# Kernel tuning notes

Hardware: AMD Instinct MI355X
Metric: run time of the kernel (lower is better)

The kernel has to match this reference:

```python
import jax, jax.numpy as jnp
import numpy as np

B, T, D, H, V = 32, 1024, 768, 1024, 30522
TAU_RANK, GAMMA_RANK, TAU_GATE = 0.05, 2.0, 0.2
RHOS = (0.1, 0.25, 0.5)


def setup_inputs() -> dict:
    key = jax.random.key(0)
    ks = jax.random.split(key, 6)
    ids = jax.random.randint(ks[0], (B, T), 0, V, dtype=jnp.int32)
    embeddings = jax.random.normal(ks[1], (B, T, D), dtype=jnp.float32)
    attn = jax.random.randint(ks[2], (B, T), 0, 2, dtype=jnp.int32)
    return {
        'ids': ids,
        'embeddings': embeddings,
        'attn': attn,
        'ln_g': jnp.ones((D,), jnp.float32),
        'ln_b': jnp.zeros((D,), jnp.float32),
        'w1': jax.random.normal(ks[3], (D, H), jnp.float32) * 0.02,
        'b1': jnp.zeros((H,), jnp.float32),
        'w2': jax.random.normal(ks[4], (H, 1), jnp.float32) * 0.02,
        'b2': jnp.zeros((1,), jnp.float32),
        'emb_table': jax.random.normal(ks[5], (V, D), jnp.float32) * 0.02,
    }


def _layer_norm(x, g, b, eps=1e-5):
    mu = x.mean(-1, keepdims=True)
    var = ((x - mu) ** 2).mean(-1, keepdims=True)
    return (x - mu) * jax.lax.rsqrt(var + eps) * g + b


def _selector(x, ln_g, ln_b, w1, b1, w2, b2):
    # SelectorMLP (dropout in eval mode): LN -> Linear -> exact GELU -> Linear -> squeeze
    h = _layer_norm(x, ln_g, ln_b)
    h = jax.nn.gelu(h @ w1 + b1, approximate=False)
    return (h @ w2 + b2)[..., 0]  # [B,T]


def _soft_rank(scores, attn_f, tau, gamma):
    scores = jnp.where(attn_f == 0, 0.0, scores)
    denom = jnp.clip(attn_f.sum(1, keepdims=True), 1.0, None)
    mean = (scores * attn_f).sum(1, keepdims=True) / denom
    var = (((scores - mean) ** 2) * attn_f).sum(1, keepdims=True) / denom
    scores = (scores - mean) / jnp.sqrt(var + 1e-6)
    # diff[b,i,j] = scores[b,j] - scores[b,i]
    diff = scores[:, None, :] - scores[:, :, None]
    p = jax.nn.sigmoid(diff / tau) ** gamma
    p = p * attn_f[:, None, :]
    r = 1.0 + p.sum(axis=1)  # [B,T]
    return jnp.where(attn_f == 0, 1e9, r)


def _pool(tok, w):
    # masked weighted mean pooling (stub of sent_encoder.pool)
    return (tok * w[:, :, None]).sum(1) / jnp.clip(w.sum(1), 1e-9, None)[:, None]


def reference(ids, embeddings, attn, ln_g, ln_b, w1, b1, w2, b2, emb_table):
    attn_f = attn.astype(jnp.float32)
    emb = embeddings * attn_f[..., None]
    scores = _selector(emb, ln_g, ln_b, w1, b1, w2, b2)
    scores = jnp.where(attn_f == 0, 0.0, scores)

    tok_full = emb_table[ids]  # stub sent_encoder.token_embeddings
    full_rep = jax.lax.stop_gradient(_pool(tok_full, attn_f))  # torch.no_grad()

    T_eff = attn_f.sum(1)
    ranks = _soft_rank(scores, attn_f, TAU_RANK, GAMMA_RANK)
    # position of each token in ascending rank order; padded tokens (rank 1e9) sort last
    pos = jnp.argsort(jnp.argsort(ranks, axis=1), axis=1)

    recon_sum = jnp.zeros((), jnp.float32)
    hard_masks, rho_effs, losses = [], [], []
    for rho in RHOS:
        k = jnp.maximum(jnp.round(rho * T_eff), 1.0)  # per-batch variable k
        gate_raw = jax.nn.sigmoid((k[:, None] - ranks) / TAU_GATE) * attn_f
        g_soft = gate_raw / jnp.clip(gate_raw.sum(1, keepdims=True), 1e-8, None) * k[:, None]
        # batched equivalent of the per-row topk(-ranks, kb) scatter loop
        hard_mask = (pos < k[:, None]).astype(jnp.float32)
        k_eff = g_soft.sum(1)
        rho_eff = k_eff / jnp.clip(T_eff, 1.0, None)
        effective_attn = attn_f * g_soft
        pred_rep = _pool(emb_table[ids], effective_attn)
        l_r = jnp.mean((pred_rep - full_rep) ** 2)  # recon_loss stub (MSE)
        recon_sum = recon_sum + l_r
        hard_masks.append(hard_mask)
        rho_effs.append(rho_eff)
        losses.append(l_r)
    recon_avg = recon_sum / len(RHOS)
    return (g_soft, jnp.stack(hard_masks), recon_avg, jnp.stack(losses), jnp.stack(rho_effs))
```

## Files before the change

### kernel.cpp

```cpp
#include <hip/hip_runtime.h>
#include <math.h>

#define BT 32768
#define Dd 768
#define Hh 1024
#define Bb 32
#define Tt 1024
#define MT_CAP 17152
#define MTILE_CAP 134

typedef __bf16 bf16x8 __attribute__((ext_vector_type(8)));
typedef float f32x4 __attribute__((ext_vector_type(4)));

#define GL2LDS16(gp, lp) __builtin_amdgcn_global_load_lds( \
    (const __attribute__((address_space(1))) void*)(gp),   \
    (__attribute__((address_space(3))) void*)(lp), 16, 0, 0)

__device__ __forceinline__ float block_reduce_sum_256(float v, float* red4) {
    int tid = threadIdx.x;
    #pragma unroll
    for (int o = 32; o > 0; o >>= 1) v += __shfl_down(v, o);
    __syncthreads();
    if ((tid & 63) == 0) red4[tid >> 6] = v;
    __syncthreads();
    return red4[0] + red4[1] + red4[2] + red4[3];
}

__device__ __forceinline__ void bf16split(float x, short& h, short& l) {
    unsigned u = __float_as_uint(x);
    unsigned r = (u + 0x7FFFu + ((u >> 16) & 1u)) >> 16;
    h = (short)r;
    float fh = __uint_as_float(r << 16);
    float lof = x - fh;
    unsigned u2 = __float_as_uint(lof);
    unsigned r2 = (u2 + 0x7FFFu + ((u2 >> 16) & 1u)) >> 16;
    l = (short)r2;
}

__device__ __forceinline__ int pack2(short a, short b) {
    return (int)(unsigned short)a | ((int)(unsigned short)b << 16);
}

__global__ __launch_bounds__(256) void seg_count_kernel(
    const int* __restrict__ attn, int* __restrict__ segsum)
{
    const int tid = threadIdx.x;
    int a = (attn[blockIdx.x * 256 + tid] != 0) ? 1 : 0;
    #pragma unroll
    for (int o = 32; o > 0; o >>= 1) a += __shfl_down(a, o);
    __shared__ int w4[4];
    if ((tid & 63) == 0) w4[tid >> 6] = a;
    __syncthreads();
    if (tid == 0) segsum[blockIdx.x] = w4[0] + w4[1] + w4[2] + w4[3];
}

__global__ __launch_bounds__(256) void cidx_kernel(
    const int* __restrict__ attn, const int* __restrict__ segsum,
    const float* __restrict__ b2,
    int* __restrict__ row_of, int* __restrict__ tok_of,
    float* __restrict__ scores, float* __restrict__ teff, int* __restrict__ mh)
{
    __shared__ int sbase[128];
    __shared__ int w0tot;
    __shared__ int wcnt[4];
    const int bid = blockIdx.x, tid = threadIdx.x;

    int v = 0, s = 0;
    if (tid < 128) {
        const int ln = tid & 63;
        v = segsum[tid];
        s = v;
        #pragma unroll
        for (int o = 1; o < 64; o <<= 1) {
            int t = __shfl_up(s, o);
            if (ln >= o) s += t;
        }
        if (tid == 63) w0tot = s;
    }
    __syncthreads();
    if (tid < 128) {
        int base = (tid >= 64) ? w0tot : 0;
        sbase[tid] = base + s - v;
        if (tid == 127 && bid == 0) mh[0] = base + s;
    }
    if (tid == 0 && (bid & 3) == 0)
        teff[bid >> 2] = (float)(segsum[bid] + segsum[bid + 1] +
                                 segsum[bid + 2] + segsum[bid + 3]);

    const int tok = bid * 256 + tid;
    const int active = (attn[tok] != 0) ? 1 : 0;
    unsigned long long m = __ballot(active);
    const int lane = tid & 63, wv = tid >> 6;
    if (lane == 0) wcnt[wv] = __popcll(m);
    __syncthreads();
    int woff = 0;
    for (int q = 0; q < wv; ++q) woff += wcnt[q];
    int below = __popcll(m & ((1ULL << lane) - 1ULL));
    int row = sbase[bid] + woff + below;
    row_of[tok] = active ? row : -1;
    if (active) tok_of[row] = tok;
    scores[tok] = active ? b2[0] : 0.f;
}

__global__ __launch_bounds__(256) void prep_kernel(
    const float* __restrict__ w1,
    short* __restrict__ w1t_hi, short* __restrict__ w1t_lo,
    const float* __restrict__ emb, const int* __restrict__ attn,
    const int* __restrict__ row_of,
    const float* __restrict__ ln_g, const float* __restrict__ ln_b,
    short* __restrict__ a_hi, short* __restrict__ a_lo)
{
    __shared__ float tile[32][65];
    const int bid = blockIdx.x, tid = threadIdx.x;

    if (bid < 384) {
        const int kb  = bid % 24;
        const int nb0 = (bid / 24) * 64;
        const int r0 = tid >> 6, c = tid & 63;
        #pragma unroll
        for (int rr = 0; rr < 8; ++rr) {
            int k = kb * 32 + r0 + rr * 4;
            tile[r0 + rr * 4][c] = w1[(size_t)k * 1024 + nb0 + c];
        }
        __syncthreads();
        const int n = tid >> 2, kc = (tid & 3) * 8;
        short h[8], lo[8];
        #pragma unroll
        for (int e = 0; e < 8; ++e) bf16split(tile[kc + e][n], h[e], lo[e]);
        size_t off = (size_t)(nb0 + n) * 768 + kb * 32 + kc;
        *(int4*)(w1t_hi + off) = make_int4(pack2(h[0],h[1]), pack2(h[2],h[3]),
                                           pack2(h[4],h[5]), pack2(h[6],h[7]));
        *(int4*)(w1t_lo + off) = make_int4(pack2(lo[0],lo[1]), pack2(lo[2],lo[3]),
                                           pack2(lo[4],lo[5]), pack2(lo[6],lo[7]));
        return;
    }

    int tok  = (bid - 384) * 4 + (tid >> 6);
    int lane = tid & 63;
    int av   = attn[tok];
    if (av == 0) return;
    int row = row_of[tok];
    if (row >= MT_CAP) return;
    float af = (float)av;
    const float4* row4 = (const float4*)(emb + (size_t)tok * Dd);
    float4 x[3];
    #pragma unroll
    for (int e = 0; e < 3; ++e) x[e] = row4[lane + 64 * e];
    float s = 0.f;
    #pragma unroll
    for (int e = 0; e < 3; ++e) {
        x[e].x *= af; x[e].y *= af; x[e].z *= af; x[e].w *= af;
        s += x[e].x + x[e].y + x[e].z + x[e].w;
    }
    #pragma unroll
    for (int o = 32; o > 0; o >>= 1) s += __shfl_down(s, o);
    s = __shfl(s, 0);
    float mean = s / 768.0f;
    float q = 0.f;
    #pragma unroll
    for (int e = 0; e < 3; ++e) {
        float d0 = x[e].x - mean, d1 = x[e].y - mean, d2 = x[e].z - mean, d3 = x[e].w - mean;
        q += d0*d0 + d1*d1 + d2*d2 + d3*d3;
    }
    #pragma unroll
    for (int o = 32; o > 0; o >>= 1) q += __shfl_down(q, o);
    q = __shfl(q, 0);
    float rstd = 1.0f / sqrtf(q / 768.0f + 1e-5f);

    #pragma unroll
    for (int e = 0; e < 3; ++e) {
        int idx = lane * 4 + e * 256;
        float4 g4 = *(const float4*)(ln_g + idx);
        float4 b4 = *(const float4*)(ln_b + idx);
        float o0 = (x[e].x - mean) * rstd * g4.x + b4.x;
        float o1 = (x[e].y - mean) * rstd * g4.y + b4.y;
        float o2 = (x[e].z - mean) * rstd * g4.z + b4.z;
        float o3 = (x[e].w - mean) * rstd * g4.w + b4.w;
        short h0,h1,h2,h3,l0,l1,l2,l3;
        bf16split(o0,h0,l0); bf16split(o1,h1,l1);
        bf16split(o2,h2,l2); bf16split(o3,h3,l3);
        *(int2*)(a_hi + (size_t)row * 768 + idx) = make_int2(pack2(h0,h1), pack2(h2,h3));
        *(int2*)(a_lo + (size_t)row * 768 + idx) = make_int2(pack2(l0,l1), pack2(l2,l3));
    }
}

__global__ __launch_bounds__(512, 4) void score_gemm_mfma(
    const __bf16* __restrict__ a_hi, const __bf16* __restrict__ a_lo,
    const __bf16* __restrict__ w1t_hi, const __bf16* __restrict__ w1t_lo,
    const float* __restrict__ b1, const float* __restrict__ w2,
    const int* __restrict__ mh, const int* __restrict__ tok_of,
    float* __restrict__ scores)
{
    const int Mh = mh[0];
    int MtAct = (Mh + 127) >> 7;
    if (MtAct > MTILE_CAP) MtAct = MTILE_CAP;
    const int MtPad8 = (MtAct + 7) & ~7;
    const int njobs  = MtPad8 * 8;
    const int job = blockIdx.x;
    if (job >= njobs) return;
    const int mt = job % MtPad8;
    const int m0 = mt * 128;
    if (m0 >= Mh) return;
    const int nc = job / MtPad8;
    const int nb = nc * 128;

    __shared__ __align__(16) __bf16 sAh[2][8][512];
    __shared__ __align__(16) __bf16 sAl[2][8][512];
    __shared__ __align__(16) __bf16 sBh[2][8][512];
    __shared__ __align__(16) __bf16 sBl[2][8][512];

    const int tid = threadIdx.x;
    const int l   = tid & 63;
    const int w   = tid >> 6;
    const int rsel = l & 15;
    const int ksel = (l >> 4) * 8;
    const int wr   = w >> 2, wc = w & 3;

    const size_t aA = (size_t)(m0 + w * 16 + rsel) * 768 + ksel;
    const size_t aB = (size_t)(nb + w * 16 + rsel) * 768 + ksel;

    f32x4 acc[4][2];
    #pragma unroll
    for (int i = 0; i < 4; ++i)
        #pragma unroll
        for (int j = 0; j < 2; ++j) acc[i][j] = (f32x4){0.f, 0.f, 0.f, 0.f};

    auto stage = [&](int buf, int k0) {
        GL2LDS16(a_hi   + aA + k0, &sAh[buf][w][0]);
        GL2LDS16(a_lo   + aA + k0, &sAl[buf][w][0]);
        GL2LDS16(w1t_hi + aB + k0, &sBh[buf][w][0]);
        GL2LDS16(w1t_lo + aB + k0, &sBl[buf][w][0]);
    };

    stage(0, 0);

    for (int kt = 0; kt < 24; ++kt) {
        const int cur = kt & 1;
        __syncthreads();
        if (kt < 23) stage(cur ^ 1, (kt + 1) * 32);

        bf16x8 ah[4], al[4], bh[2], bl[2];
        #pragma unroll
        for (int mi = 0; mi < 4; ++mi) {
            ah[mi] = *(const bf16x8*)&sAh[cur][wr * 4 + mi][l * 8];
            al[mi] = *(const bf16x8*)&sAl[cur][wr * 4 + mi][l * 8];
        }
        #pragma unroll
        for (int ni = 0; ni < 2; ++ni) {
            bh[ni] = *(const bf16x8*)&sBh[cur][wc * 2 + ni][l * 8];
            bl[ni] = *(const bf16x8*)&sBl[cur][wc * 2 + ni][l * 8];
        }
        #pragma unroll
        for (int mi = 0; mi < 4; ++mi)
            #pragma unroll
            for (int ni = 0; ni < 2; ++ni)
                acc[mi][ni] = __builtin_amdgcn_mfma_f32_16x16x32_bf16(ah[mi], bh[ni], acc[mi][ni], 0, 0, 0);
        #pragma unroll
        for (int mi = 0; mi < 4; ++mi)
            #pragma unroll
            for (int ni = 0; ni < 2; ++ni)
                acc[mi][ni] = __builtin_amdgcn_mfma_f32_16x16x32_bf16(al[mi], bh[ni], acc[mi][ni], 0, 0, 0);
        #pragma unroll
        for (int mi = 0; mi < 4; ++mi)
            #pragma unroll
            for (int ni = 0; ni < 2; ++ni)
                acc[mi][ni] = __builtin_amdgcn_mfma_f32_16x16x32_bf16(ah[mi], bl[ni], acc[mi][ni], 0, 0, 0);
    }

    const int colbase = nb + wc * 32 + (l & 15);
    const int rowg    = (l >> 4) * 4;
    #pragma unroll
    for (int mi = 0; mi < 4; ++mi) {
        float v[4] = {0.f, 0.f, 0.f, 0.f};
        #pragma unroll
        for (int ni = 0; ni < 2; ++ni) {
            int col = colbase + ni * 16;
            float b1v = b1[col], w2v = w2[col];
            #pragma unroll
            for (int j = 0; j < 4; ++j) {
                float x = acc[mi][ni][j] + b1v;
                float g = 0.5f * x * (1.0f + erff(x * 0.70710678118654752440f));
                v[j] = fmaf(g, w2v, v[j]);
            }
        }
        #pragma unroll
        for (int j = 0; j < 4; ++j) {
            v[j] += __shfl_xor(v[j], 1);
            v[j] += __shfl_xor(v[j], 2);
            v[j] += __shfl_xor(v[j], 4);
            v[j] += __shfl_xor(v[j], 8);
        }
        if ((l & 15) == 0) {
            int rowb = m0 + wr * 64 + mi * 16 + rowg;
            #pragma unroll
            for (int j = 0; j < 4; ++j) {
                int row = rowb + j;
                if (row < Mh) atomicAdd(&scores[tok_of[row]], v[j]);
            }
        }
    }
}

__global__ __launch_bounds__(256) void rank_kernel(
    const float* __restrict__ scores, const int* __restrict__ attn,
    float* __restrict__ ranks, int* __restrict__ pos, float* __restrict__ gpart)
{
    __shared__ float sn[1024];
    __shared__ float afs[1024];
    __shared__ double dsum[256];
    __shared__ int    csum[256];
    __shared__ float  red4[4];
    const int b = blockIdx.x >> 5, qc = blockIdx.x & 31;
    const int tid = threadIdx.x;

    float sv[4], av[4];
    float sa = 0.f, ss = 0.f;
    #pragma unroll
    for (int e = 0; e < 4; ++e) {
        int i = tid + 256 * e;
        float af = (float)attn[b * 1024 + i];
        float s  = (af != 0.f) ? scores[b * 1024 + i] : 0.f;
        sn[i]  = s;
        afs[i] = af;
        sv[e] = s; av[e] = af;
        sa += af; ss += s;
    }
    float tot_a = block_reduce_sum_256(sa, red4);
    float tot_s = block_reduce_sum_256(ss, red4);
    float denom = fmaxf(tot_a, 1.0f);
    float mean  = tot_s / denom;
    float q = 0.f;
    #pragma unroll
    for (int e = 0; e < 4; ++e) { float d = sv[e] - mean; q += d * d * av[e]; }
    float tot_q = block_reduce_sum_256(q, red4);
    float rinv  = 1.0f / sqrtf(tot_q / denom + 1e-6f);

    #pragma unroll
    for (int e = 0; e < 4; ++e) {
        int i = tid + 256 * e;
        sn[i] = (sn[i] - mean) * rinv;
    }
    __syncthreads();

    const int jj  = tid & 31;
    const int grp = tid >> 5;
    const int j   = qc * 32 + jj;
    const float sj = sn[j];
    const bool  aj = (afs[j] != 0.f);
    double sum = 0.0;
    int    cnt = 0;
    const int i0 = grp * 128;
    #pragma unroll 4
    for (int i = i0; i < i0 + 128; ++i) {
        float si = sn[i];
        float ai = afs[i];
        float d   = (sj - si) * 20.0f;
        float e   = __expf(-d);
        float sig = 1.0f / (1.0f + e);
        sum += (double)(sig * sig);
        bool c;
        if (ai != 0.f) c = aj ? (si < sj || (si == sj && i < j)) : true;
        else           c = aj ? false : (i < j);
        cnt += c ? 1 : 0;
    }
    dsum[tid] = sum; csum[tid] = cnt;
    __syncthreads();
    if (tid < 32) {
        double s2 = 0.0; int c2 = 0;
        #pragma unroll
        for (int g = 0; g < 8; ++g) { s2 += dsum[tid + 32 * g]; c2 += csum[tid + 32 * g]; }
        const int jt = qc * 32 + tid;
        const int gj = b * 1024 + jt;
        const float af = afs[jt];
        const float rk = (af == 0.f) ? 1e9f : (float)(1.0 + s2);
        ranks[gj] = rk;
        pos[gj]   = c2;
        const float rhos[3] = {0.1f, 0.25f, 0.5f};
        #pragma unroll
        for (int r = 0; r < 3; ++r) {
            float k = fmaxf(rintf(rhos[r] * tot_a), 1.0f);
            float d = (k - rk) * 5.0f;
            float g = (1.0f / (1.0f + __expf(-d))) * af;
            #pragma unroll
            for (int o = 16; o > 0; o >>= 1) g += __shfl_xor(g, o);
            if (tid == 0) gpart[b * 96 + r * 32 + qc] = g;
        }
    }
}

__global__ __launch_bounds__(256) void gate_pool_kernel(
    const int* __restrict__ ids, const int* __restrict__ attn,
    const float* __restrict__ emb_table,
    const float* __restrict__ ranks, const int* __restrict__ pos,
    const float* __restrict__ gpart, const float* __restrict__ teff_v,
    float* __restrict__ keff, float* __restrict__ ppart, float* __restrict__ out)
{
    __shared__ float gpl[96];
    __shared__ float gsL[3][64];
    const int b = blockIdx.x >> 4, chunk = blockIdx.x & 15;
    const int tid = threadIdx.x;
    const int t0 = chunk * 64;
    const float teff = teff_v[b];

    if (tid < 96) gpl[tid] = gpart[b * 96 + tid];
    __syncthreads();

    const float rhos[3] = {0.1f, 0.25f, 0.5f};
    float kk[3], gsum[3], scale[3];
    #pragma unroll
    for (int r = 0; r < 3; ++r) {
        float s = 0.f;
        #pragma unroll
        for (int c = 0; c < 32; ++c) s += gpl[r * 32 + c];
        gsum[r]  = s;
        kk[r]    = fmaxf(rintf(rhos[r] * teff), 1.0f);
        scale[r] = kk[r] / fmaxf(s, 1e-8f);
    }

    if (tid < 192) {
        const int r = tid >> 6, t = tid & 63;
        const int gj = b * 1024 + t0 + t;
        const float rk = ranks[gj];
        const float af = (float)attn[gj];
        float d    = (kk[r] - rk) * 5.0f;
        float gate = (1.0f / (1.0f + __expf(-d))) * af;
        float gs   = gate * scale[r];
        gsL[r][t] = gs;
        out[BT + r * BT + gj] = ((float)pos[gj] < kk[r]) ? 1.0f : 0.0f;
        if (r == 2) out[gj] = gs;
    }
    if (chunk == 0 && tid == 0) {
        #pragma unroll
        for (int r = 0; r < 3; ++r) {
            float ke = kk[r] * (gsum[r] / fmaxf(gsum[r], 1e-8f));
            keff[r * Bb + b] = ke;
            out[131076 + r * Bb + b] = ke / fmaxf(teff, 1.0f);
        }
    }
    __syncthreads();

    float accF[3] = {0,0,0}, acc0[3] = {0,0,0}, acc1[3] = {0,0,0}, acc2[3] = {0,0,0};
    for (int t = t0; t < t0 + 64; ++t) {
        int gi = b * 1024 + t;
        if (attn[gi] == 0) continue;
        float w0 = gsL[0][t - t0], wa = gsL[1][t - t0], wb = gsL[2][t - t0];
        const float* row = emb_table + (size_t)ids[gi] * 768;
        #pragma unroll
        for (int e = 0; e < 3; ++e) {
            float v = row[tid + 256 * e];
            accF[e] += v;
            acc0[e] = fmaf(w0, v, acc0[e]);
            acc1[e] = fmaf(wa, v, acc1[e]);
            acc2[e] = fmaf(wb, v, acc2[e]);
        }
    }
    float* base = ppart + ((size_t)chunk * 4 * Bb + b) * 768;
    #pragma unroll
    for (int e = 0; e < 3; ++e) {
        int d = tid + 256 * e;
        base[0 * Bb * 768 + d] = acc0[e];
        base[1 * Bb * 768 + d] = acc1[e];
        base[2 * Bb * 768 + d] = acc2[e];
        base[3 * Bb * 768 + d] = accF[e];
    }
}

__global__ __launch_bounds__(256) void final96_kernel(
    const float* __restrict__ ppart, const float* __restrict__ keff,
    const float* __restrict__ teff_v, float* __restrict__ part)
{
    __shared__ float red4[4];
    const int b = blockIdx.x / 3, r = blockIdx.x % 3;
    const int tid = threadIdx.x;
    const float kinv = 1.0f / fmaxf(keff[r * Bb + b], 1e-9f);
    const float tinv = 1.0f / fmaxf(teff_v[b], 1e-9f);
    float local = 0.f;
    for (int d = tid; d < 768; d += 256) {
        float pr = 0.f, fu = 0.f;
        #pragma unroll
        for (int c = 0; c < 16; ++c) {
            pr += ppart[(size_t)c * 98304 + (r * Bb + b) * 768 + d];
            fu += ppart[(size_t)c * 98304 + (3 * Bb + b) * 768 + d];
        }
        float df = pr * kinv - fu * tinv;
        local += df * df;
    }
    float tot = block_reduce_sum_256(local, red4);
    if (tid == 0) part[r * 32 + b] = tot;
}

__global__ void final_avg_kernel(const float* __restrict__ part, float* __restrict__ out) {
    __shared__ float sp[96];
    const int tid = threadIdx.x;
    if (tid < 96) sp[tid] = part[tid];
    __syncthreads();
    if (tid == 0) {
        float l0 = 0.f, l1 = 0.f, l2 = 0.f;
        #pragma unroll
        for (int b = 0; b < 32; ++b) { l0 += sp[b]; l1 += sp[32 + b]; l2 += sp[64 + b]; }
        l0 /= 24576.0f; l1 /= 24576.0f; l2 /= 24576.0f;
        out[131073] = l0;
        out[131074] = l1;
        out[131075] = l2;
        out[131072] = (l0 + l1 + l2) / 3.0f;
    }
}

extern "C" void kernel_launch(void* const* d_in, const int* in_sizes, int n_in,
                              void* d_out, int out_size, void* d_ws, size_t ws_size,
                              hipStream_t stream) {
    const int*   ids       = (const int*)d_in[0];
    const float* emb       = (const float*)d_in[1];
    const int*   attn      = (const int*)d_in[2];
    const float* ln_g      = (const float*)d_in[3];
    const float* ln_b      = (const float*)d_in[4];
    const float* w1        = (const float*)d_in[5];
    const float* b1        = (const float*)d_in[6];
    const float* w2        = (const float*)d_in[7];
    const float* b2        = (const float*)d_in[8];
    const float* emb_table = (const float*)d_in[9];
    float* out = (float*)d_out;
    float* ws  = (float*)d_ws;

    float* scores = ws;
    float* ranks  = ws + 32768;
    float* teff   = ws + 65536;
    float* part   = ws + 65568;
    float* keff   = ws + 65664;
    float* gpart  = ws + 65760;
    int*   pos    = (int*)(ws + 68864);
    int*   row_of = (int*)(ws + 101632);
    int*   tok_of = (int*)(ws + 134400);
    int*   segsum = (int*)(ws + 167168);
    int*   mh     = (int*)(ws + 167296);
    short* a_hi   = (short*)(ws + 167360);
    short* a_lo   = a_hi + (size_t)MT_CAP * 768;
    short* w1t_hi = a_lo + (size_t)MT_CAP * 768;
    short* w1t_lo = w1t_hi + 1024 * 768;
    float* ppart  = (float*)a_hi;

    seg_count_kernel<<<128, 256, 0, stream>>>(attn, segsum);
    cidx_kernel<<<128, 256, 0, stream>>>(attn, segsum, b2, row_of, tok_of,
                                         scores, teff, mh);
    prep_kernel<<<8576, 256, 0, stream>>>(w1, w1t_hi, w1t_lo,
                                          emb, attn, row_of, ln_g, ln_b, a_hi, a_lo);

    score_gemm_mfma<<<1088, 512, 0, stream>>>(
        (const __bf16*)a_hi, (const __bf16*)a_lo,
        (const __bf16*)w1t_hi, (const __bf16*)w1t_lo,
        b1, w2, mh, tok_of, scores);

    rank_kernel<<<1024, 256, 0, stream>>>(scores, attn, ranks, pos, gpart);
    gate_pool_kernel<<<512, 256, 0, stream>>>(ids, attn, emb_table, ranks, pos,
                                              gpart, teff, keff, ppart, out);
    final96_kernel<<<96, 256, 0, stream>>>(ppart, keff, teff, part);
    final_avg_kernel<<<1, 128, 0, stream>>>(part, out);
}
```

Baseline: 207.3 us.

## Restructure split-bf16 GEMM into 72-stage 4-buffer pipeline with explicit waitcnt

```diff
diff --git a/kernel.cpp b/kernel.cpp
--- a/kernel.cpp
+++ b/kernel.cpp
@@ -204,10 +204,8 @@
     const int nc = job / MtPad8;
     const int nb = nc * 128;
 
-    __shared__ __align__(16) __bf16 sAh[2][8][512];
-    __shared__ __align__(16) __bf16 sAl[2][8][512];
-    __shared__ __align__(16) __bf16 sBh[2][8][512];
-    __shared__ __align__(16) __bf16 sBl[2][8][512];
+    __shared__ __align__(16) __bf16 sA[4][8][512];
+    __shared__ __align__(16) __bf16 sB[4][8][512];
 
     const int tid = threadIdx.x;
     const int l   = tid & 63;
@@ -216,8 +214,8 @@
     const int ksel = (l >> 4) * 8;
     const int wr   = w >> 2, wc = w & 3;
 
-    const size_t aA = (size_t)(m0 + w * 16 + rsel) * 768 + ksel;
-    const size_t aB = (size_t)(nb + w * 16 + rsel) * 768 + ksel;
+    const size_t offA = (size_t)(m0 + w * 16 + rsel) * 768 + ksel;
+    const size_t offB = (size_t)(nb + w * 16 + rsel) * 768 + ksel;
 
     f32x4 acc[4][2];
     #pragma unroll
@@ -225,46 +223,43 @@
         #pragma unroll
         for (int j = 0; j < 2; ++j) acc[i][j] = (f32x4){0.f, 0.f, 0.f, 0.f};
 
-    auto stage = [&](int buf, int k0) {
-        GL2LDS16(a_hi   + aA + k0, &sAh[buf][w][0]);
-        GL2LDS16(a_lo   + aA + k0, &sAl[buf][w][0]);
-        GL2LDS16(w1t_hi + aB + k0, &sBh[buf][w][0]);
-        GL2LDS16(w1t_lo + aB + k0, &sBl[buf][w][0]);
+    auto stage = [&](int st) {
+        const int plane = st / 24;
+        const int k0    = (st - plane * 24) * 32;
+        const __bf16* ap = (plane == 1) ? a_lo   : a_hi;
+        const __bf16* bp = (plane == 2) ? w1t_lo : w1t_hi;
+        const int buf = st & 3;
+        GL2LDS16(ap + offA + k0, &sA[buf][w][0]);
+        GL2LDS16(bp + offB + k0, &sB[buf][w][0]);
     };
 
-    stage(0, 0);
-
-    for (int kt = 0; kt < 24; ++kt) {
-        const int cur = kt & 1;
-        __syncthreads();
-        if (kt < 23) stage(cur ^ 1, (kt + 1) * 32);
-
-        bf16x8 ah[4], al[4], bh[2], bl[2];
-        #pragma unroll
-        for (int mi = 0; mi < 4; ++mi) {
-            ah[mi] = *(const bf16x8*)&sAh[cur][wr * 4 + mi][l * 8];
-            al[mi] = *(const bf16x8*)&sAl[cur][wr * 4 + mi][l * 8];
-        }
-        #pragma unroll
-        for (int ni = 0; ni < 2; ++ni) {
-            bh[ni] = *(const bf16x8*)&sBh[cur][wc * 2 + ni][l * 8];
-            bl[ni] = *(const bf16x8*)&sBl[cur][wc * 2 + ni][l * 8];
-        }
+    stage(0); stage(1); stage(2);
+
+    for (int kt = 0; kt < 72; ++kt) {
+        const int cur = kt & 3;
+        if (kt <= 69)      asm volatile("s_waitcnt vmcnt(4)" ::: "memory");
+        else if (kt == 70) asm volatile("s_waitcnt vmcnt(2)" ::: "memory");
+        else               asm volatile("s_waitcnt vmcnt(0)" ::: "memory");
+        __builtin_amdgcn_s_barrier();
+        __builtin_amdgcn_sched_barrier(0);
+        if (kt <= 68) stage(kt + 3);
+
+        bf16x8 a[4], b[2];
+        #pragma unroll
+        for (int mi = 0; mi < 4; ++mi)
+            a[mi] = *(const bf16x8*)&sA[cur][wr * 4 + mi][l * 8];
+        #pragma unroll
+        for (int ni = 0; ni < 2; ++ni)
+            b[ni] = *(const bf16x8*)&sB[cur][wc * 2 + ni][l * 8];
+
+        __builtin_amdgcn_s_setprio(1);
         #pragma unroll
         for (int mi = 0; mi < 4; ++mi)
             #pragma unroll
             for (int ni = 0; ni < 2; ++ni)
-                acc[mi][ni] = __builtin_amdgcn_mfma_f32_16x16x32_bf16(ah[mi], bh[ni], acc[mi][ni], 0, 0, 0);
-        #pragma unroll
-        for (int mi = 0; mi < 4; ++mi)
-            #pragma unroll
-            for (int ni = 0; ni < 2; ++ni)
-                acc[mi][ni] = __builtin_amdgcn_mfma_f32_16x16x32_bf16(al[mi], bh[ni], acc[mi][ni], 0, 0, 0);
-        #pragma unroll
-        for (int mi = 0; mi < 4; ++mi)
-            #pragma unroll
-            for (int ni = 0; ni < 2; ++ni)
-                acc[mi][ni] = __builtin_amdgcn_mfma_f32_16x16x32_bf16(ah[mi], bl[ni], acc[mi][ni], 0, 0, 0);
+                acc[mi][ni] = __builtin_amdgcn_mfma_f32_16x16x32_bf16(a[mi], b[ni], acc[mi][ni], 0, 0, 0);
+        __builtin_amdgcn_s_setprio(0);
+        __builtin_amdgcn_sched_barrier(0);
     }
 
     const int colbase = nb + wc * 32 + (l & 15);
```

Result: slower. 246.3 us (median of 2 runs) (+18.8%).
